# Kernel tuning notes

Measured on AMD Instinct MI355X. Metric: run time of the kernel, lower is better.

Reference implementation:

```python
import jax, jax.numpy as jnp
import numpy as np

EPS = 1e-5
GROUPS = 128  # 4 bands * nearest_power_of_2_divisor(256, 32)

def _haar_bands(x):
    # x: (C, H, W), H and W even -> SAME pad is a no-op for 2x2 stride-2 conv.
    # lax conv is cross-correlation: band[i,j] = sum_ab x[2i+a, 2j+b] * k[a,b]
    C, H, W = x.shape
    xr = x.reshape(C, H // 2, 2, W // 2, 2)
    x00 = xr[:, :, 0, :, 0]; x01 = xr[:, :, 0, :, 1]
    x10 = xr[:, :, 1, :, 0]; x11 = xr[:, :, 1, :, 1]
    half = jnp.asarray(0.5, x.dtype)  # (1/sqrt2)^2
    LL = (x00 + x01 + x10 + x11) * half
    HL = (-x00 - x01 + x10 + x11) * half  # outer(h1, h0)
    LH = (-x00 + x01 - x10 + x11) * half  # outer(h0, h1)
    HH = (x00 - x01 - x10 + x11) * half   # outer(h1, h1)
    return LL, HL, LH, HH

def _group_norm(y, scale, bias, groups, eps=EPS):
    C, H, W = y.shape
    yg = y.reshape(groups, C // groups, H, W)
    mean = jnp.mean(yg, axis=(1, 2, 3), keepdims=True)
    var = jnp.mean(jnp.square(yg - mean), axis=(1, 2, 3), keepdims=True)
    yn = ((yg - mean) * jax.lax.rsqrt(var + eps)).reshape(C, H, W)
    return yn * scale[:, None, None] + bias[:, None, None]

def setup_inputs() -> dict:
    key = jax.random.key(0)
    k1, k2 = jax.random.split(key)
    C, H, W, Cout = 256, 256, 256, 512
    x = jax.random.normal(k1, (C, H, W), dtype=jnp.float32)
    gn_scale = jnp.ones((4 * C,), dtype=jnp.float32)
    gn_bias = jnp.zeros((4 * C,), dtype=jnp.float32)
    w_proj = jax.random.normal(k2, (Cout, 4 * C), dtype=jnp.float32) / np.sqrt(4 * C)
    return {"x": x, "gn_scale": gn_scale, "gn_bias": gn_bias, "w_proj": w_proj}

def reference(x, gn_scale, gn_bias, w_proj):
    LL, HL, LH, HH = _haar_bands(x)
    y = jnp.concatenate([LL, HL, LH, HH], axis=0)   # (4C, H/2, W/2)
    y = _group_norm(y, gn_scale, gn_bias, GROUPS)
    y = jnp.einsum('oc,chw->ohw', w_proj, y)        # 1x1 conv, no bias
    y = jax.nn.relu(y)
    # dropout p=0.0 / inference -> identity
    return y
```

## Files before the change

kernel.cpp:

```cpp
#include <hip/hip_runtime.h>
#include <stdint.h>

typedef float  f32x2 __attribute__((ext_vector_type(2)));
typedef float  f32x4 __attribute__((ext_vector_type(4)));
typedef short  s16x8 __attribute__((ext_vector_type(8)));
typedef unsigned short u16;

#define GN_EPS 1e-5f


__device__ __forceinline__ u16 f2bf(float f) {
  unsigned u = __float_as_uint(f);
  u += 0x7fffu + ((u >> 16) & 1u);
  return (u16)(u >> 16);
}

__device__ __forceinline__ float wave_red_sum(float v) {
#pragma unroll
  for (int off = 32; off > 0; off >>= 1) v += __shfl_down(v, off, 64);
  return v;
}

__device__ __forceinline__ void gload16(const void* g, void* l) {
  __builtin_amdgcn_global_load_lds(
      (const __attribute__((address_space(1))) uint32_t*)(uintptr_t)g,
      (__attribute__((address_space(3))) uint32_t*)(uintptr_t)l,
      16, 0, 0);
}

__global__ __launch_bounds__(256) void haar_kernel(
    const float* __restrict__ x, u16* __restrict__ yt,
    float* __restrict__ gsum, float* __restrict__ gsqs)
{
  const int t  = threadIdx.x;
  const int cg = blockIdx.y;
  const int hw = blockIdx.x * 256 + t;
  const int h  = hw >> 7, w = hw & 127;
  const int c0 = cg << 3;

  float s[4] = {0.f,0.f,0.f,0.f}, q[4] = {0.f,0.f,0.f,0.f};
  s16x8 ov[4];

  const float* xb = x + (size_t)(2*h) * 256 + (size_t)(2*w);
#pragma unroll
  for (int j = 0; j < 8; ++j) {
    const float* xp = xb + ((size_t)(c0 + j) << 16);
    f32x2 r0 = *(const f32x2*)(xp);
    f32x2 r1 = *(const f32x2*)(xp + 256);
    float x00 = r0.x, x01 = r0.y, x10 = r1.x, x11 = r1.y;
    float LL = 0.5f*( x00 + x01 + x10 + x11);
    float HL = 0.5f*(-x00 - x01 + x10 + x11);
    float LH = 0.5f*(-x00 + x01 - x10 + x11);
    float HH = 0.5f*( x00 - x01 - x10 + x11);
    ov[0][j] = (short)f2bf(LL);
    ov[1][j] = (short)f2bf(HL);
    ov[2][j] = (short)f2bf(LH);
    ov[3][j] = (short)f2bf(HH);
    s[0] += LL; q[0] += LL*LL;
    s[1] += HL; q[1] += HL*HL;
    s[2] += LH; q[2] += LH*LH;
    s[3] += HH; q[3] += HH*HH;
  }
  u16* yb = yt + (size_t)hw * 1024 + c0;
#pragma unroll
  for (int b = 0; b < 4; ++b)
    *(s16x8*)(yb + b*256) = ov[b];

  __shared__ float red[4][8];
  const int lane = t & 63, wv = t >> 6;
  float r[8];
#pragma unroll
  for (int j = 0; j < 8; ++j) r[j] = wave_red_sum(j < 4 ? s[j] : q[j-4]);
  if (lane == 0) {
#pragma unroll
    for (int j = 0; j < 8; ++j) red[wv][j] = r[j];
  }
  __syncthreads();
  if (t < 8) {
    float tot = red[0][t] + red[1][t] + red[2][t] + red[3][t];
    int b = t & 3;
    if (t < 4) atomicAdd(&gsum[b*32 + cg], tot);
    else       atomicAdd(&gsqs[b*32 + cg], tot);
  }
}

__global__ void stats_kernel(const float* __restrict__ gsum, const float* __restrict__ gsqs,
                             const float* __restrict__ scale, const float* __restrict__ bias,
                             float* __restrict__ ac, float* __restrict__ bc)
{
  int c = blockIdx.x * 256 + threadIdx.x;
  if (c >= 1024) return;
  int g = c >> 3;
  const float invN = 1.0f / 131072.0f;
  float mean = gsum[g] * invN;
  float var  = gsqs[g] * invN - mean * mean;
  float inv  = rsqrtf(var + GN_EPS);
  float a = scale[c] * inv;
  ac[c] = a;
  bc[c] = bias[c] - mean * a;
}

__global__ __launch_bounds__(256) void wprep_kernel(
    const float* __restrict__ wproj, const float* __restrict__ ac,
    const float* __restrict__ bc, u16* __restrict__ wn, float* __restrict__ tvec)
{
  const int o = blockIdx.x;
  const int t = threadIdx.x;
  float acc = 0.f;
#pragma unroll
  for (int j = 0; j < 4; ++j) {
    int c = j*256 + t;
    float wv = wproj[o*1024 + c];
    wn[o*1024 + c] = f2bf(wv * ac[c]);
    acc += wv * bc[c];
  }
  acc = wave_red_sum(acc);
  __shared__ float red[4];
  int lane = t & 63, wvi = t >> 6;
  if (lane == 0) red[wvi] = acc;
  __syncthreads();
  if (t == 0) tvec[o] = red[0] + red[1] + red[2] + red[3];
}

#define BM 128
#define BN 128
#define BK 64

__global__ __launch_bounds__(256) void gemm_kernel(
    const u16* __restrict__ A,
    const u16* __restrict__ B,
    const float* __restrict__ tvec,
    float* __restrict__ out)
{
  __shared__ __align__(1024) u16 As[BM*BK];
  __shared__ __align__(1024) u16 Bs[BN*BK];

  const int tid  = threadIdx.x;
  const int lane = tid & 63, wave = tid >> 6;
  const int m0 = blockIdx.y * BM;
  const int n0 = blockIdx.x * BN;
  const int wm = wave >> 1, wn_ = wave & 1;
  const int g = lane >> 4, r = lane & 15;

  f32x4 acc[4][4];
#pragma unroll
  for (int i = 0; i < 4; ++i)
#pragma unroll
    for (int j = 0; j < 4; ++j) acc[i][j] = (f32x4)(0.f);

  for (int k0 = 0; k0 < 1024; k0 += BK) {
#pragma unroll
    for (int ci = 0; ci < 4; ++ci) {
      int chunk  = wave*4 + ci;
      int linear = chunk*1024 + lane*16;
      int row    = linear >> 7;
      int sb     = linear & 127;
      int so     = sb ^ ((row & 7) << 4);
      gload16((const char*)(A + (size_t)(m0 + row)*1024 + k0) + so,
              (char*)As + chunk*1024);
      gload16((const char*)(B + (size_t)(n0 + row)*1024 + k0) + so,
              (char*)Bs + chunk*1024);
    }
    __syncthreads();

#pragma unroll
    for (int kk = 0; kk < 2; ++kk) {
      s16x8 av[4], bv[4];
      const int kb = g*16 + kk*64;
#pragma unroll
      for (int m = 0; m < 4; ++m) {
        int row = wm*64 + m*16 + r;
        av[m] = *(const s16x8*)((const char*)As + row*128 + (kb ^ ((row & 7) << 4)));
      }
#pragma unroll
      for (int n = 0; n < 4; ++n) {
        int row = wn_*64 + n*16 + r;
        bv[n] = *(const s16x8*)((const char*)Bs + row*128 + (kb ^ ((row & 7) << 4)));
      }
#pragma unroll
      for (int m = 0; m < 4; ++m)
#pragma unroll
        for (int n = 0; n < 4; ++n)
          acc[m][n] = __builtin_amdgcn_mfma_f32_16x16x32_bf16(av[m], bv[n], acc[m][n], 0, 0, 0);
    }
    __syncthreads();
  }

#pragma unroll
  for (int m = 0; m < 4; ++m) {
#pragma unroll
    for (int rr = 0; rr < 4; ++rr) {
      int o = m0 + wm*64 + m*16 + g*4 + rr;
      float tv = tvec[o];
      float* op = out + (size_t)o*16384 + n0 + wn_*64 + r;
#pragma unroll
      for (int n = 0; n < 4; ++n) {
        float v = acc[m][n][rr] + tv;
        op[n*16] = v > 0.f ? v : 0.f;
      }
    }
  }
}

extern "C" void kernel_launch(void* const* d_in, const int* in_sizes, int n_in,
                              void* d_out, int out_size, void* d_ws, size_t ws_size,
                              hipStream_t stream)
{
  const float* x  = (const float*)d_in[0];
  const float* sc = (const float*)d_in[1];
  const float* bi = (const float*)d_in[2];
  const float* wp = (const float*)d_in[3];
  float* out = (float*)d_out;

  char* ws = (char*)d_ws;
  float* gsum = (float*)(ws + 0);
  float* gsqs = (float*)(ws + 512);
  float* ac   = (float*)(ws + 1024);
  float* bc   = (float*)(ws + 5120);
  float* tv   = (float*)(ws + 9216);
  u16*   wn   = (u16*)(ws + 16384);
  u16*   yt   = (u16*)(ws + 2097152);

  hipMemsetAsync(ws, 0, 1024, stream);
  hipLaunchKernelGGL(haar_kernel,  dim3(64, 32), dim3(256), 0, stream, x, yt, gsum, gsqs);
  hipLaunchKernelGGL(stats_kernel, dim3(4),      dim3(256), 0, stream, gsum, gsqs, sc, bi, ac, bc);
  hipLaunchKernelGGL(wprep_kernel, dim3(512),    dim3(256), 0, stream, wp, ac, bc, wn, tv);
  hipLaunchKernelGGL(gemm_kernel,  dim3(128, 4), dim3(256), 0, stream, wn, yt, tv, out);
}
```

Baseline: 161.9 us.

## Restructure haar thread mapping, fold stats into wprep, remap GEMM blocks for XCDs

The haar kernel now gives each thread two adjacent output pixels across 8 channels, using 16-byte input loads. Eight channel-lanes per pixel group write contiguous 16-byte chunks of the transposed bf16 output, so stores coalesce better. The separate stats kernel is removed: its group-norm coefficient computation now runs inside wprep, which saves one launch but repeats the rsqrt work per output row. The GEMM grid is flattened and block IDs are remapped so blocks on the same XCD share B tiles, aiming at better L2 reuse.

```diff
diff --git a/kernel.cpp b/kernel.cpp
--- a/kernel.cpp
+++ b/kernel.cpp
@@ -32,87 +32,99 @@
     const float* __restrict__ x, u16* __restrict__ yt,
     float* __restrict__ gsum, float* __restrict__ gsqs)
 {
-  const int t  = threadIdx.x;
-  const int cg = blockIdx.y;
-  const int hw = blockIdx.x * 256 + t;
-  const int h  = hw >> 7, w = hw & 127;
-  const int c0 = cg << 3;
-
-  float s[4] = {0.f,0.f,0.f,0.f}, q[4] = {0.f,0.f,0.f,0.f};
-  s16x8 ov[4];
-
-  const float* xb = x + (size_t)(2*h) * 256 + (size_t)(2*w);
+  const int t    = threadIdx.x;
+  const int cti  = t & 7;
+  const int hwi  = t >> 3;
+  const int hw0  = blockIdx.x * 64 + hwi * 2;
+  const int h    = hw0 >> 7, w = hw0 & 127;
+  const int cin0 = blockIdx.y * 64 + cti * 8;
+
+  float sv[4] = {0.f,0.f,0.f,0.f}, qv[4] = {0.f,0.f,0.f,0.f};
+  s16x8 ov[2][4];
+
+  const float* xb = x + ((size_t)cin0 << 16) + (size_t)(2*h)*256 + (size_t)(2*w);
 #pragma unroll
   for (int j = 0; j < 8; ++j) {
-    const float* xp = xb + ((size_t)(c0 + j) << 16);
-    f32x2 r0 = *(const f32x2*)(xp);
-    f32x2 r1 = *(const f32x2*)(xp + 256);
-    float x00 = r0.x, x01 = r0.y, x10 = r1.x, x11 = r1.y;
-    float LL = 0.5f*( x00 + x01 + x10 + x11);
-    float HL = 0.5f*(-x00 - x01 + x10 + x11);
-    float LH = 0.5f*(-x00 + x01 - x10 + x11);
-    float HH = 0.5f*( x00 - x01 - x10 + x11);
-    ov[0][j] = (short)f2bf(LL);
-    ov[1][j] = (short)f2bf(HL);
-    ov[2][j] = (short)f2bf(LH);
-    ov[3][j] = (short)f2bf(HH);
-    s[0] += LL; q[0] += LL*LL;
-    s[1] += HL; q[1] += HL*HL;
-    s[2] += LH; q[2] += LH*LH;
-    s[3] += HH; q[3] += HH*HH;
-  }
-  u16* yb = yt + (size_t)hw * 1024 + c0;
-#pragma unroll
-  for (int b = 0; b < 4; ++b)
-    *(s16x8*)(yb + b*256) = ov[b];
-
-  __shared__ float red[4][8];
+    const float* xp = xb + ((size_t)j << 16);
+    f32x4 r0 = *(const f32x4*)(xp);
+    f32x4 r1 = *(const f32x4*)(xp + 256);
+#pragma unroll
+    for (int p = 0; p < 2; ++p) {
+      float x00 = p ? r0.z : r0.x;
+      float x01 = p ? r0.w : r0.y;
+      float x10 = p ? r1.z : r1.x;
+      float x11 = p ? r1.w : r1.y;
+      float LL = 0.5f*( x00 + x01 + x10 + x11);
+      float HL = 0.5f*(-x00 - x01 + x10 + x11);
+      float LH = 0.5f*(-x00 + x01 - x10 + x11);
+      float HH = 0.5f*( x00 - x01 - x10 + x11);
+      ov[p][0][j] = (short)f2bf(LL);
+      ov[p][1][j] = (short)f2bf(HL);
+      ov[p][2][j] = (short)f2bf(LH);
+      ov[p][3][j] = (short)f2bf(HH);
+      sv[0] += LL; qv[0] += LL*LL;
+      sv[1] += HL; qv[1] += HL*HL;
+      sv[2] += LH; qv[2] += LH*LH;
+      sv[3] += HH; qv[3] += HH*HH;
+    }
+  }
+
+  u16* yb = yt + (size_t)hw0 * 1024 + cin0;
+#pragma unroll
+  for (int p = 0; p < 2; ++p)
+#pragma unroll
+    for (int b = 0; b < 4; ++b)
+      *(s16x8*)(yb + p*1024 + b*256) = ov[p][b];
+
+#pragma unroll
+  for (int k = 0; k < 4; ++k) {
+#pragma unroll
+    for (int msk = 8; msk < 64; msk <<= 1) {
+      sv[k] += __shfl_xor(sv[k], msk, 64);
+      qv[k] += __shfl_xor(qv[k], msk, 64);
+    }
+  }
+  __shared__ float red[4][8][8];
   const int lane = t & 63, wv = t >> 6;
-  float r[8];
-#pragma unroll
-  for (int j = 0; j < 8; ++j) r[j] = wave_red_sum(j < 4 ? s[j] : q[j-4]);
-  if (lane == 0) {
-#pragma unroll
-    for (int j = 0; j < 8; ++j) red[wv][j] = r[j];
+  if (lane < 8) {
+#pragma unroll
+    for (int k = 0; k < 4; ++k) {
+      red[wv][lane][k]     = sv[k];
+      red[wv][lane][4 + k] = qv[k];
+    }
   }
   __syncthreads();
-  if (t < 8) {
-    float tot = red[0][t] + red[1][t] + red[2][t] + red[3][t];
-    int b = t & 3;
-    if (t < 4) atomicAdd(&gsum[b*32 + cg], tot);
-    else       atomicAdd(&gsqs[b*32 + cg], tot);
-  }
-}
-
-__global__ void stats_kernel(const float* __restrict__ gsum, const float* __restrict__ gsqs,
-                             const float* __restrict__ scale, const float* __restrict__ bias,
-                             float* __restrict__ ac, float* __restrict__ bc)
-{
-  int c = blockIdx.x * 256 + threadIdx.x;
-  if (c >= 1024) return;
-  int g = c >> 3;
-  const float invN = 1.0f / 131072.0f;
-  float mean = gsum[g] * invN;
-  float var  = gsqs[g] * invN - mean * mean;
-  float inv  = rsqrtf(var + GN_EPS);
-  float a = scale[c] * inv;
-  ac[c] = a;
-  bc[c] = bias[c] - mean * a;
+  if (t < 64) {
+    int c8 = t & 7, vi = t >> 3;
+    float tot = red[0][c8][vi] + red[1][c8][vi] + red[2][c8][vi] + red[3][c8][vi];
+    int b = vi & 3;
+    int g = b*32 + blockIdx.y*8 + c8;
+    if (vi < 4) atomicAdd(&gsum[g], tot);
+    else        atomicAdd(&gsqs[g], tot);
+  }
 }
 
 __global__ __launch_bounds__(256) void wprep_kernel(
-    const float* __restrict__ wproj, const float* __restrict__ ac,
-    const float* __restrict__ bc, u16* __restrict__ wn, float* __restrict__ tvec)
+    const float* __restrict__ wproj, const float* __restrict__ gsum,
+    const float* __restrict__ gsqs, const float* __restrict__ scale,
+    const float* __restrict__ bias, u16* __restrict__ wn, float* __restrict__ tvec)
 {
   const int o = blockIdx.x;
   const int t = threadIdx.x;
+  const float invN = 1.0f / 131072.0f;
   float acc = 0.f;
 #pragma unroll
   for (int j = 0; j < 4; ++j) {
     int c = j*256 + t;
+    int g = c >> 3;
+    float mean = gsum[g] * invN;
+    float var  = gsqs[g] * invN - mean * mean;
+    float inv  = rsqrtf(var + GN_EPS);
+    float a = scale[c] * inv;
+    float b = bias[c] - mean * a;
     float wv = wproj[o*1024 + c];
-    wn[o*1024 + c] = f2bf(wv * ac[c]);
-    acc += wv * bc[c];
+    wn[o*1024 + c] = f2bf(wv * a);
+    acc += wv * b;
   }
   acc = wave_red_sum(acc);
   __shared__ float red[4];
@@ -137,8 +149,12 @@
 
   const int tid  = threadIdx.x;
   const int lane = tid & 63, wave = tid >> 6;
-  const int m0 = blockIdx.y * BM;
-  const int n0 = blockIdx.x * BN;
+
+  const int bid = blockIdx.x;
+  const int cid = (bid & 7) * 64 + (bid >> 3);
+  const int m0 = (cid & 3) * BM;
+  const int n0 = (cid >> 2) * BN;
+
   const int wm = wave >> 1, wn_ = wave & 1;
   const int g = lane >> 4, r = lane & 15;
 
@@ -215,15 +231,12 @@
   char* ws = (char*)d_ws;
   float* gsum = (float*)(ws + 0);
   float* gsqs = (float*)(ws + 512);
-  float* ac   = (float*)(ws + 1024);
-  float* bc   = (float*)(ws + 5120);
   float* tv   = (float*)(ws + 9216);
   u16*   wn   = (u16*)(ws + 16384);
   u16*   yt   = (u16*)(ws + 2097152);
 
   hipMemsetAsync(ws, 0, 1024, stream);
-  hipLaunchKernelGGL(haar_kernel,  dim3(64, 32), dim3(256), 0, stream, x, yt, gsum, gsqs);
-  hipLaunchKernelGGL(stats_kernel, dim3(4),      dim3(256), 0, stream, gsum, gsqs, sc, bi, ac, bc);
-  hipLaunchKernelGGL(wprep_kernel, dim3(512),    dim3(256), 0, stream, wp, ac, bc, wn, tv);
-  hipLaunchKernelGGL(gemm_kernel,  dim3(128, 4), dim3(256), 0, stream, wn, yt, tv, out);
-}
+  hipLaunchKernelGGL(haar_kernel,  dim3(256, 4), dim3(256), 0, stream, x, yt, gsum, gsqs);
+  hipLaunchKernelGGL(wprep_kernel, dim3(512),    dim3(256), 0, stream, wp, gsum, gsqs, sc, bi, wn, tv);
+  hipLaunchKernelGGL(gemm_kernel,  dim3(512),    dim3(256), 0, stream, wn, yt, tv, out);
+}
```

Result: faster. 142.1 us (-12.2%).
